# Kernel tuning notes

Measured on AMD Instinct MI355X. Metric: run time of the kernel, lower is better.

Reference implementation:

```python
import jax, jax.numpy as jnp
import numpy as np

H = 16         # num query heads
KV = 8         # num kv heads
HD = 64        # head_dim
WINDOW = 512   # sliding window size
ROPE_BASE = 10000.0


def rotate_half(x):
    x1, x2 = x[..., : x.shape[-1] // 2], x[..., x.shape[-1] // 2 :]
    return jnp.concatenate((-x2, x1), axis=-1)


def rope_cos_sin(seq_len, dim, dtype):
    inv_freq = 1.0 / (ROPE_BASE ** (jnp.arange(0, dim, 2, dtype=jnp.float32) / dim))
    t = jnp.arange(seq_len, dtype=jnp.float32)
    freqs = jnp.outer(t, inv_freq)              # [S, dim/2]
    emb = jnp.concatenate((freqs, freqs), axis=-1)  # [S, dim]
    return jnp.cos(emb).astype(dtype), jnp.sin(emb).astype(dtype)


def setup_inputs() -> dict:
    key = jax.random.key(0)
    ks = jax.random.split(key, 5)
    B, S, D = 2, 2048, 1024
    std = 0.02
    return {
        "hidden_states": jax.random.normal(ks[0], (B, S, D), dtype=jnp.float32),
        "Wq": jax.random.normal(ks[1], (D, H * HD), dtype=jnp.float32) * std,
        "Wk": jax.random.normal(ks[2], (D, KV * HD), dtype=jnp.float32) * std,
        "Wv": jax.random.normal(ks[3], (D, KV * HD), dtype=jnp.float32) * std,
        "Wo": jax.random.normal(ks[4], (H * HD, D), dtype=jnp.float32) * std,
    }


def reference(hidden_states, Wq, Wk, Wv, Wo):
    B, S, D = hidden_states.shape
    n_rep = H // KV

    q = (hidden_states @ Wq).reshape(B, S, H, HD).transpose(0, 2, 1, 3)   # [B,H,S,hd]
    k = (hidden_states @ Wk).reshape(B, S, KV, HD).transpose(0, 2, 1, 3)  # [B,KV,S,hd]
    v = (hidden_states @ Wv).reshape(B, S, KV, HD).transpose(0, 2, 1, 3)

    cos, sin = rope_cos_sin(S, HD, q.dtype)  # [S,hd]
    cos = cos[None, None]
    sin = sin[None, None]
    q = q * cos + rotate_half(q) * sin
    k = k * cos + rotate_half(k) * sin

    # repeat kv heads for GQA ([:, :, None] expand + reshape == repeat along head axis)
    k = jnp.repeat(k, n_rep, axis=1)  # [B,H,S,hd]
    v = jnp.repeat(v, n_rep, axis=1)

    scores = jnp.einsum("bhqd,bhkd->bhqk", q, k) / jnp.sqrt(jnp.asarray(HD, q.dtype))
    i = jnp.arange(S)[:, None]
    j = jnp.arange(S)[None, :]
    allowed = (j <= i) & (j >= i - WINDOW)  # causal + sliding window
    scores = jnp.where(allowed[None, None], scores, -jnp.inf)

    attn = jax.nn.softmax(scores, axis=-1)
    out = jnp.einsum("bhqk,bhkd->bhqd", attn, v)          # [B,H,S,hd]
    out = out.transpose(0, 2, 1, 3).reshape(B, S, H * HD)  # [B,S,D]
    return out @ Wo
```

## Files before the change

### kernel.cpp

```cpp
#include <hip/hip_runtime.h>
#include <hip/hip_bf16.h>

typedef __attribute__((ext_vector_type(8))) short short8;
typedef __attribute__((ext_vector_type(4))) float f32x4;

#define S_LEN 2048
#define NH 16
#define NKV 8
#define HD 64
#define WIN 512
#define DMODEL 1024
#define LOG2_10000 13.287712379549449f

#define GLOAD16(g, l)                                                        \
    __builtin_amdgcn_global_load_lds(                                        \
        (const __attribute__((address_space(1))) unsigned int*)(g),          \
        (__attribute__((address_space(3))) unsigned int*)(l), 16, 0, 0)

__global__ void cast_bf16_kernel(const float* __restrict__ X,
                                 __hip_bfloat16* __restrict__ Y, int n) {
    int i = (blockIdx.x * 256 + threadIdx.x) * 4;
    if (i + 3 < n) {
        float4 v = *reinterpret_cast<const float4*>(X + i);
        Y[i + 0] = __float2bfloat16(v.x);
        Y[i + 1] = __float2bfloat16(v.y);
        Y[i + 2] = __float2bfloat16(v.z);
        Y[i + 3] = __float2bfloat16(v.w);
    }
}

__global__ void transpose_cast4_kernel(const float* __restrict__ W0,
                                       const float* __restrict__ W1,
                                       const float* __restrict__ W2,
                                       const float* __restrict__ W3,
                                       __hip_bfloat16* __restrict__ WqkvT,
                                       __hip_bfloat16* __restrict__ WoT) {
    __shared__ float tile[32][33];
    const int K = DMODEL;
    const float* W;
    __hip_bfloat16* WT;
    int N;
    switch (blockIdx.z) {
        case 0: W = W0; WT = WqkvT;                          N = 1024; break;
        case 1: W = W1; WT = WqkvT + (size_t)1024 * K;       N = 512;  break;
        case 2: W = W2; WT = WqkvT + (size_t)1536 * K;       N = 512;  break;
        default: W = W3; WT = WoT;                           N = 1024; break;
    }
    if ((int)blockIdx.x * 32 >= N) return;
    int nx = blockIdx.x * 32 + threadIdx.x;
    int k0 = blockIdx.y * 32;
#pragma unroll
    for (int r = 0; r < 4; ++r) {
        int k = k0 + threadIdx.y + r * 8;
        tile[threadIdx.y + r * 8][threadIdx.x] = W[(size_t)k * N + nx];
    }
    __syncthreads();
#pragma unroll
    for (int r = 0; r < 4; ++r) {
        int nn = blockIdx.x * 32 + threadIdx.y + r * 8;
        int kk = k0 + threadIdx.x;
        WT[(size_t)nn * K + kk] = __float2bfloat16(tile[threadIdx.x][threadIdx.y + r * 8]);
    }
}

template <int MODE>
__global__ __launch_bounds__(128) void gemm128_kernel(
    const __hip_bfloat16* __restrict__ A,
    const __hip_bfloat16* __restrict__ BT,
    void* __restrict__ o0, void* __restrict__ o1, void* __restrict__ o2,
    int N, int K) {
    __shared__ __hip_bfloat16 ldsA[2][128 * 32];
    __shared__ __hip_bfloat16 ldsB[2][64 * 32];
    const int tx = threadIdx.x;
    const int wave = tx >> 6;
    const int lane = tx & 63;
    const int l16 = lane & 15;
    const int quad = lane >> 4;
    const int col0 = blockIdx.x * 64;
    const int row0 = blockIdx.y * 128;
    const int wrow = wave * 64;

    f32x4 acc[4][4] = {};

    const int arow = tx >> 2;
    const int kc8 = (tx & 3) * 8;
    const __hip_bfloat16* gA = A + (size_t)(row0 + arow) * K + kc8;
    const __hip_bfloat16* gB = BT + (size_t)(col0 + arow) * K + kc8;

    auto stage = [&](int k0, int bf) {
        char* lA = (char*)(&ldsA[bf][0]) + tx * 16;
        char* lB = (char*)(&ldsB[bf][0]) + tx * 16;
#pragma unroll
        for (int r = 0; r < 4; ++r)
            GLOAD16(gA + (size_t)(r * 32) * K + k0, lA + r * 2048);
#pragma unroll
        for (int r = 0; r < 2; ++r)
            GLOAD16(gB + (size_t)(r * 32) * K + k0, lB + r * 2048);
    };

    stage(0, 0);
    int buf = 0;
    for (int k0 = 0; k0 < K; k0 += 32) {
        __syncthreads();
        if (k0 + 32 < K) stage(k0 + 32, buf ^ 1);
        short8 af[4], bf4[4];
#pragma unroll
        for (int i = 0; i < 4; ++i) {
            af[i] = *reinterpret_cast<const short8*>(
                &ldsA[buf][0] + (wrow + i * 16 + l16) * 32 + quad * 8);
            bf4[i] = *reinterpret_cast<const short8*>(
                &ldsB[buf][0] + (i * 16 + l16) * 32 + quad * 8);
        }
#pragma unroll
        for (int mi = 0; mi < 4; ++mi)
#pragma unroll
            for (int ni = 0; ni < 4; ++ni)
                acc[mi][ni] = __builtin_amdgcn_mfma_f32_16x16x32_bf16(
                    af[mi], bf4[ni], acc[mi][ni], 0, 0, 0);
        buf ^= 1;
    }

    const int rbase = row0 + wrow;
    if (MODE == 0) {
        const int cbaseg = col0;
        const bool isQ = (cbaseg < DMODEL);
        const bool isK = (cbaseg >= DMODEL) && (cbaseg < DMODEL + 512);
        if (isQ || isK) {
            float invf[2];
            invf[0] = exp2f(-(float)(l16)      * (LOG2_10000 / 32.0f));
            invf[1] = exp2f(-(float)(16 + l16) * (LOG2_10000 / 32.0f));
#pragma unroll
            for (int mi = 0; mi < 4; ++mi)
#pragma unroll
                for (int r = 0; r < 4; ++r) {
                    int srow = (rbase + mi * 16 + quad * 4 + r) & (S_LEN - 1);
#pragma unroll
                    for (int ni = 0; ni < 2; ++ni) {
                        float ang = (float)srow * invf[ni];
                        float c = __cosf(ang), s = __sinf(ang);
                        float x1 = acc[mi][ni][r], x2 = acc[mi][ni + 2][r];
                        acc[mi][ni][r]     = x1 * c - x2 * s;
                        acc[mi][ni + 2][r] = x2 * c + x1 * s;
                    }
                }
            __hip_bfloat16* Co = (__hip_bfloat16*)(isQ ? o0 : o1);
            int cbase = isQ ? cbaseg : cbaseg - DMODEL;
            int rowstride = isQ ? (NH * HD) : (NKV * HD);
#pragma unroll
            for (int mi = 0; mi < 4; ++mi)
#pragma unroll
                for (int ni = 0; ni < 4; ++ni) {
                    size_t col = cbase + ni * 16 + l16;
#pragma unroll
                    for (int r = 0; r < 4; ++r)
                        Co[(size_t)(rbase + mi * 16 + quad * 4 + r) * rowstride + col] =
                            __float2bfloat16(acc[mi][ni][r]);
                }
        } else {
            __hip_bfloat16* VTo = (__hip_bfloat16*)o2;
            int bb = row0 >> 11;
#pragma unroll
            for (int mi = 0; mi < 4; ++mi) {
                int s = ((rbase + mi * 16 + quad * 4) & (S_LEN - 1));
#pragma unroll
                for (int ni = 0; ni < 4; ++ni) {
                    int colv = cbaseg - 1536 + ni * 16 + l16;
                    int vh = colv >> 6, d = colv & 63;
                    alignas(8) __hip_bfloat16 hv[4];
#pragma unroll
                    for (int r = 0; r < 4; ++r) hv[r] = __float2bfloat16(acc[mi][ni][r]);
                    *reinterpret_cast<ushort4*>(
                        VTo + ((size_t)(bb * NKV + vh) * HD + d) * S_LEN + s) =
                        *reinterpret_cast<ushort4*>(hv);
                }
            }
        }
    } else {
        float* Co = (float*)o0;
#pragma unroll
        for (int mi = 0; mi < 4; ++mi)
#pragma unroll
            for (int ni = 0; ni < 4; ++ni) {
                size_t col = col0 + ni * 16 + l16;
#pragma unroll
                for (int r = 0; r < 4; ++r)
                    Co[(size_t)(rbase + mi * 16 + quad * 4 + r) * N + col] = acc[mi][ni][r];
            }
    }
}

__global__ __launch_bounds__(256, 4) void attn_mfma_kernel(
    const __hip_bfloat16* __restrict__ Q,
    const __hip_bfloat16* __restrict__ K,
    const __hip_bfloat16* __restrict__ VT,
    __hip_bfloat16* __restrict__ O) {
    __shared__ __hip_bfloat16 ldsK[2][64][64];
    __shared__ __hip_bfloat16 ldsVT[2][64][64];
    __shared__ __hip_bfloat16 ldsP[4][16][64];
    const int tx = threadIdx.x;
    const int wave = tx >> 6;
    const int lane = tx & 63;
    const int l16 = lane & 15;
    const int quad = lane >> 4;
    const int q0 = blockIdx.x * 64;
    const int h = blockIdx.y;
    const int kvh = h >> 1;
    const int b = blockIdx.z;
    const int qi = q0 + wave * 16 + l16;

    short8 aq[2];
    {
        const __hip_bfloat16* qp =
            Q + (size_t)(b * S_LEN + qi) * (NH * HD) + h * HD + quad * 8;
        aq[0] = *reinterpret_cast<const short8*>(qp);
        aq[1] = *reinterpret_cast<const short8*>(qp + 32);
    }
    f32x4 acc_o[4] = {};
    float m = -1e30f, l = 0.f;
    const float SL2 = 0.125f * 1.4426950408889634f;

    const int s_row = tx >> 3;
    const int s_c8 = (((tx & 7) ^ (s_row & 7))) * 8;
    const int sw = (l16 & 7);
    auto stage = [&](int j0, int bf) {
        char* lk = (char*)(&ldsK[bf][0][0]) + tx * 16;
        char* lv = (char*)(&ldsVT[bf][0][0]) + tx * 16;
#pragma unroll
        for (int r = 0; r < 2; ++r) {
            int row = s_row + r * 32;
            GLOAD16(K + (size_t)(b * S_LEN + j0 + row) * (NKV * HD) + kvh * HD + s_c8,
                    lk + r * 4096);
            GLOAD16(VT + ((size_t)(b * NKV + kvh) * HD + row) * S_LEN + j0 + s_c8,
                    lv + r * 4096);
        }
    };

    const int kstart = (q0 >= WIN) ? (q0 - WIN) : 0;
    stage(kstart, 0);
    int buf = 0;

    char* prow = (char*)(&ldsP[wave][l16][0]);

    for (int j0 = kstart; j0 <= q0; j0 += 64) {
        __syncthreads();
        if (j0 + 64 <= q0) stage(j0 + 64, buf ^ 1);

        f32x4 sacc[4] = {};
#pragma unroll
        for (int t = 0; t < 4; ++t) {
            const __hip_bfloat16* krow = &ldsK[buf][t * 16 + l16][0];
            short8 bk0 = *reinterpret_cast<const short8*>(krow + ((quad ^ sw) * 8));
            short8 bk1 = *reinterpret_cast<const short8*>(krow + (((4 + quad) ^ sw) * 8));
            sacc[t] = __builtin_amdgcn_mfma_f32_16x16x32_bf16(bk0, aq[0], sacc[t], 0, 0, 0);
            sacc[t] = __builtin_amdgcn_mfma_f32_16x16x32_bf16(bk1, aq[1], sacc[t], 0, 0, 0);
        }

        const bool need_mask = (j0 == q0) || (q0 >= WIN && j0 == kstart);
        float sv[4][4];
        if (need_mask) {
#pragma unroll
            for (int t = 0; t < 4; ++t)
#pragma unroll
                for (int r = 0; r < 4; ++r) {
                    int j = j0 + t * 16 + quad * 4 + r;
                    bool ok = (j <= qi) && (j + WIN >= qi);
                    sv[t][r] = ok ? sacc[t][r] * SL2 : -1e30f;
                }
        } else {
#pragma unroll
            for (int t = 0; t < 4; ++t)
#pragma unroll
                for (int r = 0; r < 4; ++r) sv[t][r] = sacc[t][r] * SL2;
        }
        float cm = -1e30f;
#pragma unroll
        for (int t = 0; t < 4; ++t)
#pragma unroll
            for (int r = 0; r < 4; ++r) cm = fmaxf(cm, sv[t][r]);
        cm = fmaxf(cm, __shfl_xor(cm, 16));
        cm = fmaxf(cm, __shfl_xor(cm, 32));
        float mn = fmaxf(m, cm);
        float alpha = exp2f(m - mn);
        m = mn;
        float sp = 0.f;
#pragma unroll
        for (int t = 0; t < 4; ++t)
#pragma unroll
            for (int r = 0; r < 4; ++r) { sv[t][r] = exp2f(sv[t][r] - mn); sp += sv[t][r]; }
        sp += __shfl_xor(sp, 16);
        sp += __shfl_xor(sp, 32);
        l = l * alpha + sp;
#pragma unroll
        for (int t = 0; t < 4; ++t)
#pragma unroll
            for (int r = 0; r < 4; ++r) acc_o[t][r] *= alpha;
#pragma unroll
        for (int t = 0; t < 4; ++t) {
            alignas(8) __hip_bfloat16 hp[4];
#pragma unroll
            for (int r = 0; r < 4; ++r) hp[r] = __float2bfloat16(sv[t][r]);
            int swb = ((((2 * t + (quad >> 1)) ^ (l16 & 7)) << 4) | ((quad & 1) << 3));
            *reinterpret_cast<ushort4*>(prow + swb) = *reinterpret_cast<ushort4*>(hp);
        }

#pragma unroll
        for (int ks = 0; ks < 2; ++ks) {
            short8 pf = *reinterpret_cast<const short8*>(
                prow + (((4 * ks + quad) ^ (l16 & 7)) << 4));
#pragma unroll
            for (int t = 0; t < 4; ++t) {
                const __hip_bfloat16* vrow = &ldsVT[buf][t * 16 + l16][0];
                short8 vf = *reinterpret_cast<const short8*>(
                    vrow + (((ks * 4 + quad) ^ sw) * 8));
                acc_o[t] = __builtin_amdgcn_mfma_f32_16x16x32_bf16(vf, pf, acc_o[t], 0, 0, 0);
            }
        }
        buf ^= 1;
    }

    {
        float inv = 1.f / l;
        __hip_bfloat16* op =
            O + (size_t)(b * S_LEN + qi) * (NH * HD) + h * HD;
#pragma unroll
        for (int t = 0; t < 4; ++t) {
            alignas(8) __hip_bfloat16 ho[4];
#pragma unroll
            for (int r = 0; r < 4; ++r) ho[r] = __float2bfloat16(acc_o[t][r] * inv);
            *reinterpret_cast<ushort4*>(op + t * 16 + quad * 4) =
                *reinterpret_cast<ushort4*>(ho);
        }
    }
}

extern "C" void kernel_launch(void* const* d_in, const int* in_sizes, int n_in,
                              void* d_out, int out_size, void* d_ws, size_t ws_size,
                              hipStream_t stream) {
    const float* X  = (const float*)d_in[0];
    const float* Wq = (const float*)d_in[1];
    const float* Wk = (const float*)d_in[2];
    const float* Wv = (const float*)d_in[3];
    const float* Wo = (const float*)d_in[4];
    float* out = (float*)d_out;

    const int ROWS = 2 * S_LEN;
    char* ws = (char*)d_ws;
    size_t off = 0;
    __hip_bfloat16* Xb     = (__hip_bfloat16*)(ws + off); off += (size_t)ROWS * DMODEL * 2;
    __hip_bfloat16* WqkvT  = (__hip_bfloat16*)(ws + off); off += (size_t)2048 * DMODEL * 2;
    __hip_bfloat16* WoT    = (__hip_bfloat16*)(ws + off); off += (size_t)DMODEL * DMODEL * 2;
    __hip_bfloat16* Qb     = (__hip_bfloat16*)(ws + off); off += (size_t)ROWS * (NH * HD) * 2;
    __hip_bfloat16* Kb     = (__hip_bfloat16*)(ws + off); off += (size_t)ROWS * (NKV * HD) * 2;
    __hip_bfloat16* VTg    = (__hip_bfloat16*)(ws + off); off += (size_t)ROWS * (NKV * HD) * 2;
    __hip_bfloat16* Ob     = (__hip_bfloat16*)(ws + off); off += (size_t)ROWS * (NH * HD) * 2;

    cast_bf16_kernel<<<(ROWS * DMODEL) / (256 * 4), 256, 0, stream>>>(X, Xb, ROWS * DMODEL);
    transpose_cast4_kernel<<<dim3(32, 32, 4), dim3(32, 8), 0, stream>>>(
        Wq, Wk, Wv, Wo, WqkvT, WoT);

    gemm128_kernel<0><<<dim3(2048 / 64, ROWS / 128), 128, 0, stream>>>(
        Xb, WqkvT, Qb, Kb, VTg, 2048, DMODEL);

    attn_mfma_kernel<<<dim3(S_LEN / 64, NH, 2), 256, 0, stream>>>(Qb, Kb, VTg, Ob);

    gemm128_kernel<1><<<dim3(DMODEL / 64, ROWS / 128), 128, 0, stream>>>(
        Ob, WoT, out, nullptr, nullptr, DMODEL, DMODEL);
}
```

Baseline: 161.9 us.

## Fuse prep kernels, use 4-wave GEMM blocks, and skip rescale in attention

Merges the input cast and weight transpose into one prep launch with vectorized bf16 stores. The GEMM now runs 256 threads per block, each wave owning 32 rows, which cuts per-thread accumulators and staging loads to raise occupancy. Attention skips the running-max update and the accumulator rescale unless the new max exceeds the old by more than 8 in log2 units. That lazy rescale lets the unnormalized exponentials grow up to 2^8, a small numeric risk.

```diff
diff --git a/kernel.cpp b/kernel.cpp
--- a/kernel.cpp
+++ b/kernel.cpp
@@ -17,24 +17,31 @@
         (const __attribute__((address_space(1))) unsigned int*)(g),          \
         (__attribute__((address_space(3))) unsigned int*)(l), 16, 0, 0)
 
-__global__ void cast_bf16_kernel(const float* __restrict__ X,
-                                 __hip_bfloat16* __restrict__ Y, int n) {
-    int i = (blockIdx.x * 256 + threadIdx.x) * 4;
-    if (i + 3 < n) {
-        float4 v = *reinterpret_cast<const float4*>(X + i);
-        Y[i + 0] = __float2bfloat16(v.x);
-        Y[i + 1] = __float2bfloat16(v.y);
-        Y[i + 2] = __float2bfloat16(v.z);
-        Y[i + 3] = __float2bfloat16(v.w);
-    }
-}
-
-__global__ void transpose_cast4_kernel(const float* __restrict__ W0,
-                                       const float* __restrict__ W1,
-                                       const float* __restrict__ W2,
-                                       const float* __restrict__ W3,
-                                       __hip_bfloat16* __restrict__ WqkvT,
-                                       __hip_bfloat16* __restrict__ WoT) {
+__global__ void prep_kernel(const float* __restrict__ X,
+                            const float* __restrict__ W0,
+                            const float* __restrict__ W1,
+                            const float* __restrict__ W2,
+                            const float* __restrict__ W3,
+                            __hip_bfloat16* __restrict__ Xb,
+                            __hip_bfloat16* __restrict__ WqkvT,
+                            __hip_bfloat16* __restrict__ WoT) {
+    if (blockIdx.z == 4) {
+        int tid = (blockIdx.y * 32 + blockIdx.x) * 256 + threadIdx.y * 32 + threadIdx.x;
+        const float4* Xi = reinterpret_cast<const float4*>(X);
+#pragma unroll
+        for (int r = 0; r < 4; ++r) {
+            int i = tid + r * (1024 * 256);
+            float4 v = Xi[i];
+            alignas(8) __hip_bfloat16 h[4];
+            h[0] = __float2bfloat16(v.x);
+            h[1] = __float2bfloat16(v.y);
+            h[2] = __float2bfloat16(v.z);
+            h[3] = __float2bfloat16(v.w);
+            *reinterpret_cast<ushort4*>(Xb + (size_t)i * 4) =
+                *reinterpret_cast<ushort4*>(h);
+        }
+        return;
+    }
     __shared__ float tile[32][33];
     const int K = DMODEL;
     const float* W;
@@ -64,7 +71,7 @@
 }
 
 template <int MODE>
-__global__ __launch_bounds__(128) void gemm128_kernel(
+__global__ __launch_bounds__(256, 4) void gemm128_kernel(
     const __hip_bfloat16* __restrict__ A,
     const __hip_bfloat16* __restrict__ BT,
     void* __restrict__ o0, void* __restrict__ o1, void* __restrict__ o2,
@@ -78,9 +85,9 @@
     const int quad = lane >> 4;
     const int col0 = blockIdx.x * 64;
     const int row0 = blockIdx.y * 128;
-    const int wrow = wave * 64;
-
-    f32x4 acc[4][4] = {};
+    const int wrow = wave * 32;
+
+    f32x4 acc[2][4] = {};
 
     const int arow = tx >> 2;
     const int kc8 = (tx & 3) * 8;
@@ -90,12 +97,9 @@
     auto stage = [&](int k0, int bf) {
         char* lA = (char*)(&ldsA[bf][0]) + tx * 16;
         char* lB = (char*)(&ldsB[bf][0]) + tx * 16;
-#pragma unroll
-        for (int r = 0; r < 4; ++r)
-            GLOAD16(gA + (size_t)(r * 32) * K + k0, lA + r * 2048);
-#pragma unroll
-        for (int r = 0; r < 2; ++r)
-            GLOAD16(gB + (size_t)(r * 32) * K + k0, lB + r * 2048);
+        GLOAD16(gA + k0, lA);
+        GLOAD16(gA + (size_t)64 * K + k0, lA + 4096);
+        GLOAD16(gB + k0, lB);
     };
 
     stage(0, 0);
@@ -103,16 +107,17 @@
     for (int k0 = 0; k0 < K; k0 += 32) {
         __syncthreads();
         if (k0 + 32 < K) stage(k0 + 32, buf ^ 1);
-        short8 af[4], bf4[4];
-#pragma unroll
-        for (int i = 0; i < 4; ++i) {
+        short8 af[2], bf4[4];
+#pragma unroll
+        for (int i = 0; i < 2; ++i)
             af[i] = *reinterpret_cast<const short8*>(
                 &ldsA[buf][0] + (wrow + i * 16 + l16) * 32 + quad * 8);
+#pragma unroll
+        for (int i = 0; i < 4; ++i)
             bf4[i] = *reinterpret_cast<const short8*>(
                 &ldsB[buf][0] + (i * 16 + l16) * 32 + quad * 8);
-        }
-#pragma unroll
-        for (int mi = 0; mi < 4; ++mi)
+#pragma unroll
+        for (int mi = 0; mi < 2; ++mi)
 #pragma unroll
             for (int ni = 0; ni < 4; ++ni)
                 acc[mi][ni] = __builtin_amdgcn_mfma_f32_16x16x32_bf16(
@@ -130,7 +135,7 @@
             invf[0] = exp2f(-(float)(l16)      * (LOG2_10000 / 32.0f));
             invf[1] = exp2f(-(float)(16 + l16) * (LOG2_10000 / 32.0f));
 #pragma unroll
-            for (int mi = 0; mi < 4; ++mi)
+            for (int mi = 0; mi < 2; ++mi)
 #pragma unroll
                 for (int r = 0; r < 4; ++r) {
                     int srow = (rbase + mi * 16 + quad * 4 + r) & (S_LEN - 1);
@@ -147,7 +152,7 @@
             int cbase = isQ ? cbaseg : cbaseg - DMODEL;
             int rowstride = isQ ? (NH * HD) : (NKV * HD);
 #pragma unroll
-            for (int mi = 0; mi < 4; ++mi)
+            for (int mi = 0; mi < 2; ++mi)
 #pragma unroll
                 for (int ni = 0; ni < 4; ++ni) {
                     size_t col = cbase + ni * 16 + l16;
@@ -160,7 +165,7 @@
             __hip_bfloat16* VTo = (__hip_bfloat16*)o2;
             int bb = row0 >> 11;
 #pragma unroll
-            for (int mi = 0; mi < 4; ++mi) {
+            for (int mi = 0; mi < 2; ++mi) {
                 int s = ((rbase + mi * 16 + quad * 4) & (S_LEN - 1));
 #pragma unroll
                 for (int ni = 0; ni < 4; ++ni) {
@@ -178,7 +183,7 @@
     } else {
         float* Co = (float*)o0;
 #pragma unroll
-        for (int mi = 0; mi < 4; ++mi)
+        for (int mi = 0; mi < 2; ++mi)
 #pragma unroll
             for (int ni = 0; ni < 4; ++ni) {
                 size_t col = col0 + ni * 16 + l16;
@@ -279,21 +284,24 @@
             for (int r = 0; r < 4; ++r) cm = fmaxf(cm, sv[t][r]);
         cm = fmaxf(cm, __shfl_xor(cm, 16));
         cm = fmaxf(cm, __shfl_xor(cm, 32));
-        float mn = fmaxf(m, cm);
-        float alpha = exp2f(m - mn);
-        m = mn;
+        if (!__all(cm - m <= 8.0f)) {
+            float mn = fmaxf(m, cm);
+            float alpha = exp2f(m - mn);
+            m = mn;
+            l *= alpha;
+#pragma unroll
+            for (int t = 0; t < 4; ++t)
+#pragma unroll
+                for (int r = 0; r < 4; ++r) acc_o[t][r] *= alpha;
+        }
         float sp = 0.f;
 #pragma unroll
         for (int t = 0; t < 4; ++t)
 #pragma unroll
-            for (int r = 0; r < 4; ++r) { sv[t][r] = exp2f(sv[t][r] - mn); sp += sv[t][r]; }
+            for (int r = 0; r < 4; ++r) { sv[t][r] = exp2f(sv[t][r] - m); sp += sv[t][r]; }
         sp += __shfl_xor(sp, 16);
         sp += __shfl_xor(sp, 32);
-        l = l * alpha + sp;
-#pragma unroll
-        for (int t = 0; t < 4; ++t)
-#pragma unroll
-            for (int r = 0; r < 4; ++r) acc_o[t][r] *= alpha;
+        l += sp;
 #pragma unroll
         for (int t = 0; t < 4; ++t) {
             alignas(8) __hip_bfloat16 hp[4];
@@ -354,15 +362,14 @@
     __hip_bfloat16* VTg    = (__hip_bfloat16*)(ws + off); off += (size_t)ROWS * (NKV * HD) * 2;
     __hip_bfloat16* Ob     = (__hip_bfloat16*)(ws + off); off += (size_t)ROWS * (NH * HD) * 2;
 
-    cast_bf16_kernel<<<(ROWS * DMODEL) / (256 * 4), 256, 0, stream>>>(X, Xb, ROWS * DMODEL);
-    transpose_cast4_kernel<<<dim3(32, 32, 4), dim3(32, 8), 0, stream>>>(
-        Wq, Wk, Wv, Wo, WqkvT, WoT);
-
-    gemm128_kernel<0><<<dim3(2048 / 64, ROWS / 128), 128, 0, stream>>>(
+    prep_kernel<<<dim3(32, 32, 5), dim3(32, 8), 0, stream>>>(
+        X, Wq, Wk, Wv, Wo, Xb, WqkvT, WoT);
+
+    gemm128_kernel<0><<<dim3(2048 / 64, ROWS / 128), 256, 0, stream>>>(
         Xb, WqkvT, Qb, Kb, VTg, 2048, DMODEL);
 
     attn_mfma_kernel<<<dim3(S_LEN / 64, NH, 2), 256, 0, stream>>>(Qb, Kb, VTg, Ob);
 
-    gemm128_kernel<1><<<dim3(DMODEL / 64, ROWS / 128), 128, 0, stream>>>(
+    gemm128_kernel<1><<<dim3(DMODEL / 64, ROWS / 128), 256, 0, stream>>>(
         Ob, WoT, out, nullptr, nullptr, DMODEL, DMODEL);
 }
```

Measured after the change: 158.5 us. 2.1% less time.
